# Optimization experiments

Hardware: AMD Instinct MI355X
Metric: run time of the kernel (lower is better)

The kernel has to match this reference:

```python
import jax, jax.numpy as jnp
import numpy as np

INPUT_DIM = 2048
LATENT_DIM = 16384
K = 64
BATCH = 8192


def setup_inputs() -> dict:
    key = jax.random.key(0)
    kx, kw, kbe, kbd = jax.random.split(key, 4)
    x = jax.random.normal(kx, (BATCH, INPUT_DIM), dtype=jnp.float32)
    # torch nn.Linear default init: U(-1/sqrt(fan_in), 1/sqrt(fan_in))
    lim_e = 1.0 / np.sqrt(INPUT_DIM)
    W_enc = jax.random.uniform(kw, (LATENT_DIM, INPUT_DIM), minval=-lim_e, maxval=lim_e, dtype=jnp.float32)
    b_enc = jax.random.uniform(kbe, (LATENT_DIM,), minval=-lim_e, maxval=lim_e, dtype=jnp.float32)
    # decoder weight tied at init to encoder.weight.T -> shape [INPUT_DIM, LATENT_DIM]
    W_dec = W_enc.T
    lim_d = 1.0 / np.sqrt(LATENT_DIM)
    b_dec = jax.random.uniform(kbd, (INPUT_DIM,), minval=-lim_d, maxval=lim_d, dtype=jnp.float32)
    return {"x": x, "W_enc": W_enc, "b_enc": b_enc, "W_dec": W_dec, "b_dec": b_dec}


def reference(x, W_enc, b_enc, W_dec, b_dec):
    # encode: [B, D] @ [D, L] + [L] -> [B, L]
    pre_acts = jax.nn.relu(x @ W_enc.T + b_enc)
    # top-k over latent dim
    topk_vals, topk_idx = jax.lax.top_k(pre_acts, K)          # [B, K]
    # scatter top-k values into a zero latent tensor
    rows = jnp.arange(pre_acts.shape[0])[:, None]             # [B, 1]
    z = jnp.zeros_like(pre_acts).at[rows, topk_idx].set(topk_vals)
    # decode: [B, L] @ [L, D] + [D]
    x_hat = z @ W_dec.T + b_dec
    return (x_hat, z)
```

## Files before the change

kernel.cpp:

```cpp
#include <hip/hip_runtime.h>
#include <cstdint>
#include <cstddef>


#define BATCH  8192
#define IN_DIM 2048
#define LAT    16384
#define TOPK   64

typedef __attribute__((ext_vector_type(8))) _Float16  f16x8;
typedef __attribute__((ext_vector_type(4))) _Float16  f16x4;
typedef __attribute__((ext_vector_type(4))) float     f32x4;
typedef __attribute__((ext_vector_type(8))) unsigned short us8;

#define GLOAD16(gp, lp) __builtin_amdgcn_global_load_lds(                     \
    (const __attribute__((address_space(1))) void*)(gp),                      \
    (__attribute__((address_space(3))) void*)(lp), 16, 0, 0)

__global__ __launch_bounds__(256) void conv_tile(
    const float* __restrict__ X, const float* __restrict__ Wm,
    _Float16* __restrict__ Xt, _Float16* __restrict__ Wt,
    _Float16* __restrict__ Wd)
{
  __shared__ _Float16 l[4096];
  const int t = blockIdx.x;
  const float* src;
  _Float16* dst;
  int grow0 = -1, gcol0 = 0;
  if (t < 4096) {
    src = X + ((size_t)(t >> 6) * 128) * IN_DIM + (t & 63) * 32;
    dst = Xt + (size_t)t * 4096;
  } else {
    const int u = t - 4096;
    src = Wm + ((size_t)(u >> 6) * 128) * IN_DIM + (u & 63) * 32;
    dst = Wt + (size_t)u * 4096;
    grow0 = (u >> 6) * 128;
    gcol0 = (u & 63) * 32;
  }
  const int tid = threadIdx.x;
#pragma unroll
  for (int i = 0; i < 4; ++i) {
    const int q = tid + i * 256;
    const int row = q >> 3, f4 = q & 7;
    const float4 v = *reinterpret_cast<const float4*>(src + (size_t)row * IN_DIM + f4 * 4);
    f16x4 hv;
    hv[0] = (_Float16)v.x; hv[1] = (_Float16)v.y;
    hv[2] = (_Float16)v.z; hv[3] = (_Float16)v.w;
    *reinterpret_cast<f16x4*>(&l[(f4 >> 1) * 1024 + row * 8 + (f4 & 1) * 4]) = hv;
    if (grow0 >= 0)
      *reinterpret_cast<f16x4*>(
          &Wd[(size_t)(grow0 + row) * IN_DIM + gcol0 + f4 * 4]) = hv;
  }
  __syncthreads();
#pragma unroll
  for (int i = 0; i < 2; ++i) {
    const int q = tid + i * 256;
    *reinterpret_cast<us8*>(&dst[(size_t)q * 8]) =
        *reinterpret_cast<const us8*>(&l[q * 8]);
  }
}

#define WAITV(N) asm volatile("s_waitcnt vmcnt(" #N ")" ::: "memory")
#define WAITL do { asm volatile("s_waitcnt lgkmcnt(0)" ::: "memory");         \
                   __builtin_amdgcn_sched_barrier(0); } while (0)
#define BAR __builtin_amdgcn_s_barrier()

#define STAGE_A(par, bufus, t1) do {                                          \
  GLOAD16(At + ((size_t)(bm * 2 + 0) * 64 + 2 * (t1) + (par)) * 4096 + tid8,  \
          &lds[(bufus) + (par) * 8192 + tid8]);                               \
  GLOAD16(At + ((size_t)(bm * 2 + 1) * 64 + 2 * (t1) + (par)) * 4096 + tid8,  \
          &lds[(bufus) + (par) * 8192 + 4096 + tid8]);                        \
} while (0)
#define STAGE_B(par, bufus, t1) do {                                          \
  GLOAD16(Bt + ((size_t)(bn * 2 + 0) * 64 + 2 * (t1) + (par)) * 4096 + tid8,  \
          &lds[(bufus) + 16384 + (par) * 8192 + tid8]);                       \
  GLOAD16(Bt + ((size_t)(bn * 2 + 1) * 64 + 2 * (t1) + (par)) * 4096 + tid8,  \
          &lds[(bufus) + 16384 + (par) * 8192 + 4096 + tid8]);                \
} while (0)

#define LDA4(D, par, bufus, fbase) do {                                       \
  const int _b = (bufus) + (par) * 8192 + wr * 4096 + kg * 1024 + r16 * 8;    \
  _Pragma("unroll") for (int f = 0; f < 4; ++f)                               \
    D[f] = *reinterpret_cast<const f16x8*>(&lds[_b + ((fbase) + f) * 128]);   \
} while (0)
#define LDB4(D, par, bufus) do {                                              \
  const int _b = (bufus) + 16384 + (par) * 8192 + (wc >> 1) * 4096            \
               + kg * 1024 + (wc & 1) * 512 + r16 * 8;                        \
  _Pragma("unroll") for (int g = 0; g < 4; ++g)                               \
    D[g] = *reinterpret_cast<const f16x8*>(&lds[_b + g * 128]);               \
} while (0)

#define MFMA16(fbase, A4, B4) do {                                            \
  __builtin_amdgcn_s_setprio(1);                                              \
  _Pragma("unroll") for (int f = 0; f < 4; ++f)                               \
    _Pragma("unroll") for (int g = 0; g < 4; ++g)                             \
      acc[(fbase) + f][g] = __builtin_amdgcn_mfma_f32_16x16x32_f16(           \
          A4[f], B4[g], acc[(fbase) + f][g], 0, 0, 0);                        \
  __builtin_amdgcn_s_setprio(0); } while (0)

__global__ __launch_bounds__(512, 2) void encode_f16(
    const _Float16* __restrict__ At,
    const _Float16* __restrict__ Bt,
    const float* __restrict__ bias,
    float* __restrict__ C)
{
  __shared__ _Float16 lds[65536];
  const int tid  = threadIdx.x;
  const int lane = tid & 63, wid = tid >> 6;
  const int wr = wid >> 2, wc = wid & 3;
  const int r16 = lane & 15, kg = lane >> 4;
  const int tid8 = tid * 8;

  const int bid = blockIdx.x;
  const int swz = (bid & 7) * 256 + (bid >> 3);
  const int bn = swz & 63, bm = swz >> 6;

  f32x4 acc[8][4];
#pragma unroll
  for (int i = 0; i < 8; ++i)
#pragma unroll
    for (int j = 0; j < 4; ++j) acc[i][j] = (f32x4)0.f;

  f16x8 a0[4], a1[4], bb[4];

  STAGE_A(0, 0, 0);
  STAGE_B(0, 0, 0);
  STAGE_A(1, 0, 0);
  STAGE_B(1, 0, 0);
  WAITV(4);
  BAR;

#pragma unroll 2
  for (int t = 0; t < 31; ++t) {
    const int cur = (t & 1) * 32768, nxt = cur ^ 32768;
    LDA4(a0, 0, cur, 0);
    LDB4(bb, 0, cur);
    STAGE_A(0, nxt, t + 1);
    BAR; WAITL;
    MFMA16(0, a0, bb);
    BAR;
    LDA4(a1, 0, cur, 4);
    STAGE_B(0, nxt, t + 1);
    WAITV(4);
    BAR; WAITL;
    MFMA16(4, a1, bb);
    BAR;
    LDA4(a0, 1, cur, 0);
    LDB4(bb, 1, cur);
    STAGE_A(1, nxt, t + 1);
    STAGE_B(1, nxt, t + 1);
    BAR; WAITL;
    MFMA16(0, a0, bb);
    BAR;
    LDA4(a1, 1, cur, 4);
    WAITV(4);
    BAR; WAITL;
    MFMA16(4, a1, bb);
    BAR;
  }

  {
    const int cur = 32768;
    LDA4(a0, 0, cur, 0);
    LDB4(bb, 0, cur);
    BAR; WAITL;
    MFMA16(0, a0, bb);
    BAR;
    LDA4(a1, 0, cur, 4);
    WAITV(0);
    BAR; WAITL;
    MFMA16(4, a1, bb);
    BAR;
    LDA4(a0, 1, cur, 0);
    LDB4(bb, 1, cur);
    BAR; WAITL;
    MFMA16(0, a0, bb);
    BAR;
    LDA4(a1, 1, cur, 4);
    WAITL;
    MFMA16(4, a1, bb);
  }

  const int row0 = bm * 256 + wr * 128 + (lane >> 4) * 4;
  const int col0 = bn * 256 + wc * 64 + r16;
#pragma unroll
  for (int fj = 0; fj < 4; ++fj) {
    const float bv = bias[col0 + fj * 16];
#pragma unroll
    for (int fi = 0; fi < 8; ++fi) {
#pragma unroll
      for (int q = 0; q < 4; ++q) {
        const float tv = acc[fi][fj][q] + bv;
        C[(size_t)(row0 + fi * 16 + q) * LAT + col0 + fj * 16] = tv > 0.f ? tv : 0.f;
      }
    }
  }
}

#define REFINE_WIN 0.01f
#define MAXMID 96

__global__ __launch_bounds__(256) void topk_decode(
    float* __restrict__ Z,
    const float* __restrict__ X,
    const float* __restrict__ Wm,
    const float* __restrict__ benc,
    const _Float16* __restrict__ Wd,
    const float* __restrict__ b_dec,
    float* __restrict__ Xhat)
{
  const int row = blockIdx.x;
  const int tid = threadIdx.x;
  float* zrow = Z + (size_t)row * LAT;
  const float* xrow = X + (size_t)row * IN_DIM;

  float v[64];
#pragma unroll
  for (int i = 0; i < 16; ++i) {
    const float4 t = *reinterpret_cast<const float4*>(&zrow[(tid << 2) + (i << 10)]);
    v[i * 4 + 0] = t.x; v[i * 4 + 1] = t.y; v[i * 4 + 2] = t.z; v[i * 4 + 3] = t.w;
  }

  __shared__ int hist[256];
  __shared__ int sbuf[256];
  __shared__ int s_bin, s_krnext;
  uint32_t prefix = 0, mask = 0;
  int kr = TOPK;
  for (int p = 3; p >= 2; --p) {
    hist[tid] = 0;
    __syncthreads();
#pragma unroll
    for (int i = 0; i < 64; ++i) {
      const uint32_t u = __float_as_uint(v[i]);
      if ((u & mask) == prefix) atomicAdd(&hist[(u >> (p * 8)) & 255], 1);
    }
    __syncthreads();
    sbuf[tid] = hist[tid];
    for (int s = 1; s < 256; s <<= 1) {
      __syncthreads();
      const int y = (tid + s < 256) ? sbuf[tid + s] : 0;
      __syncthreads();
      sbuf[tid] += y;
    }
    __syncthreads();
    const int suf  = sbuf[tid];
    const int sufn = (tid < 255) ? sbuf[tid + 1] : 0;
    if (suf >= kr && sufn < kr) { s_bin = tid; s_krnext = kr - sufn; }
    __syncthreads();
    prefix |= (uint32_t)s_bin << (p * 8);
    mask   |= 0xFFu << (p * 8);
    kr = s_krnext;
    __syncthreads();
  }

  const float blo = __uint_as_float(prefix);
  const float bhi = __uint_as_float(prefix + 0x10000u);
  const float thi = bhi + REFINE_WIN;
  const float wlo = blo - REFINE_WIN;

  __shared__ int   s_cnt, s_mc;
  __shared__ int   s_mi[MAXMID];
  __shared__ float s_mv[MAXMID];
  __shared__ int   s_oi[TOPK];
  __shared__ float s_ov[TOPK];
  if (tid == 0) { s_cnt = 0; s_mc = 0; }
  __syncthreads();

#pragma unroll
  for (int i = 0; i < 16; ++i) {
    const int ebase = (tid << 2) + (i << 10);
    float4 ov;
    float* op = reinterpret_cast<float*>(&ov);
#pragma unroll
    for (int q = 0; q < 4; ++q) {
      const float val = v[i * 4 + q];
      float o = 0.f;
      if (val > thi) {
        o = val;
        const int pz = atomicAdd(&s_cnt, 1);
        s_oi[pz] = ebase + q;
        s_ov[pz] = val;
      } else if (val >= wlo) {
        const int pe = atomicAdd(&s_mc, 1);
        if (pe < MAXMID) { s_mi[pe] = ebase + q; s_mv[pe] = val; }
      }
      op[q] = o;
    }
    *reinterpret_cast<float4*>(&zrow[ebase]) = ov;
  }
  __syncthreads();

  const int mc = (s_mc < MAXMID) ? s_mc : MAXMID;
  const int m  = TOPK - s_cnt;

  __shared__ double s_ev[MAXMID];
  {
    const int wv = tid >> 6, ln = tid & 63;
    for (int j = wv; j < mc; j += 4) {
      const float* wr = Wm + (size_t)s_mi[j] * IN_DIM;
      const int k0 = ln * 32;
      double p = 0.0;
#pragma unroll
      for (int k = 0; k < 32; ++k)
        p = fma((double)xrow[k0 + k], (double)wr[k0 + k], p);
#pragma unroll
      for (int s = 32; s > 0; s >>= 1) p += __shfl_xor(p, s);
      if (ln == 0) s_ev[j] = p + (double)benc[s_mi[j]];
    }
  }
  __syncthreads();

  if (tid == 0) {
    const int base = s_cnt;
    for (int r = 0; r < m; ++r) {
      int bj = -1;
      for (int j = 0; j < mc; ++j) {
        if (s_ev[j] < -1e290) continue;
        if (bj < 0 || s_ev[j] > s_ev[bj] ||
            (s_ev[j] == s_ev[bj] && s_mi[j] < s_mi[bj])) bj = j;
      }
      if (bj < 0) break;
      zrow[s_mi[bj]] = s_mv[bj];
      s_oi[base + r] = s_mi[bj];
      s_ov[base + r] = s_mv[bj];
      s_ev[bj] = -1e300;
    }
  }
  __syncthreads();

  const int d = tid * 8;
  float4 acc0 = *reinterpret_cast<const float4*>(&b_dec[d]);
  float4 acc1 = *reinterpret_cast<const float4*>(&b_dec[d + 4]);
#pragma unroll 4
  for (int k = 0; k < TOPK; ++k) {
    const float s = s_ov[k];
    const f16x8 wv8 = *reinterpret_cast<const f16x8*>(
        &Wd[(size_t)s_oi[k] * IN_DIM + d]);
    acc0.x = fmaf(s, (float)wv8[0], acc0.x);
    acc0.y = fmaf(s, (float)wv8[1], acc0.y);
    acc0.z = fmaf(s, (float)wv8[2], acc0.z);
    acc0.w = fmaf(s, (float)wv8[3], acc0.w);
    acc1.x = fmaf(s, (float)wv8[4], acc1.x);
    acc1.y = fmaf(s, (float)wv8[5], acc1.y);
    acc1.z = fmaf(s, (float)wv8[6], acc1.z);
    acc1.w = fmaf(s, (float)wv8[7], acc1.w);
  }
  float* xp = &Xhat[(size_t)row * IN_DIM + d];
  *reinterpret_cast<float4*>(xp) = acc0;
  *reinterpret_cast<float4*>(xp + 4) = acc1;
}

constexpr int BMf = 128, BNf = 128, BKf = 16;

__global__ __launch_bounds__(256) void encode_gemm_f64(
    const float* __restrict__ A, const float* __restrict__ B,
    const float* __restrict__ bias, float* __restrict__ C)
{
  __shared__ float As[BKf][BMf + 4];
  __shared__ float Bs[BKf][BNf + 4];
  const int tid = threadIdx.x;
  const int tx = tid & 15, ty = tid >> 4;
  const int block_n = blockIdx.x * BNf, block_m = blockIdx.y * BMf;
  double acc[8][8];
#pragma unroll
  for (int i = 0; i < 8; ++i)
#pragma unroll
    for (int j = 0; j < 8; ++j) acc[i][j] = 0.0;
  const int lr = tid >> 2, lc = tid & 3;
  for (int k0 = 0; k0 < IN_DIM; k0 += BKf) {
    __syncthreads();
#pragma unroll
    for (int it = 0; it < 2; ++it) {
      const int r = lr + it * 64;
      const float4 va = *reinterpret_cast<const float4*>(&A[(size_t)(block_m + r) * IN_DIM + k0 + lc * 4]);
      As[lc * 4 + 0][r] = va.x; As[lc * 4 + 1][r] = va.y;
      As[lc * 4 + 2][r] = va.z; As[lc * 4 + 3][r] = va.w;
      const float4 vb = *reinterpret_cast<const float4*>(&B[(size_t)(block_n + r) * IN_DIM + k0 + lc * 4]);
      Bs[lc * 4 + 0][r] = vb.x; Bs[lc * 4 + 1][r] = vb.y;
      Bs[lc * 4 + 2][r] = vb.z; Bs[lc * 4 + 3][r] = vb.w;
    }
    __syncthreads();
#pragma unroll
    for (int k = 0; k < BKf; ++k) {
      const float4 a0 = *reinterpret_cast<const float4*>(&As[k][ty * 8]);
      const float4 a1 = *reinterpret_cast<const float4*>(&As[k][ty * 8 + 4]);
      const float4 b0 = *reinterpret_cast<const float4*>(&Bs[k][tx * 8]);
      const float4 b1 = *reinterpret_cast<const float4*>(&Bs[k][tx * 8 + 4]);
      const double a[8] = {(double)a0.x, (double)a0.y, (double)a0.z, (double)a0.w,
                           (double)a1.x, (double)a1.y, (double)a1.z, (double)a1.w};
      const double b[8] = {(double)b0.x, (double)b0.y, (double)b0.z, (double)b0.w,
                           (double)b1.x, (double)b1.y, (double)b1.z, (double)b1.w};
#pragma unroll
      for (int i = 0; i < 8; ++i)
#pragma unroll
        for (int j = 0; j < 8; ++j) acc[i][j] = fma(a[i], b[j], acc[i][j]);
    }
  }
  float bv[8];
#pragma unroll
  for (int j = 0; j < 8; ++j) bv[j] = bias[block_n + tx * 8 + j];
#pragma unroll
  for (int i = 0; i < 8; ++i) {
    const int row = block_m + ty * 8 + i;
    float o[8];
#pragma unroll
    for (int j = 0; j < 8; ++j) {
      const double s = acc[i][j] + (double)bv[j];
      o[j] = (float)(s > 0.0 ? s : 0.0);
    }
    float* cp = &C[(size_t)row * LAT + block_n + tx * 8];
    *reinterpret_cast<float4*>(cp)     = make_float4(o[0], o[1], o[2], o[3]);
    *reinterpret_cast<float4*>(cp + 4) = make_float4(o[4], o[5], o[6], o[7]);
  }
}

__global__ __launch_bounds__(256) void topk_fallback(
    float* __restrict__ Z, const float* __restrict__ X,
    const float* __restrict__ Wm, const float* __restrict__ benc,
    int* __restrict__ idx_out, float* __restrict__ val_out)
{
  const int row = blockIdx.x;
  const int tid = threadIdx.x;
  float* zrow = Z + (size_t)row * LAT;
  const float* xrow = X + (size_t)row * IN_DIM;
  float v[64];
#pragma unroll
  for (int i = 0; i < 16; ++i) {
    const float4 t = *reinterpret_cast<const float4*>(&zrow[(tid << 2) + (i << 10)]);
    v[i * 4 + 0] = t.x; v[i * 4 + 1] = t.y; v[i * 4 + 2] = t.z; v[i * 4 + 3] = t.w;
  }
  __shared__ int hist[256];
  __shared__ int sbuf[256];
  __shared__ int s_bin, s_krnext;
  uint32_t prefix = 0, mask = 0;
  int kr = TOPK;
  for (int p = 3; p >= 0; --p) {
    hist[tid] = 0;
    __syncthreads();
#pragma unroll
    for (int i = 0; i < 64; ++i) {
      const uint32_t u = __float_as_uint(v[i]);
      if ((u & mask) == prefix) atomicAdd(&hist[(u >> (p * 8)) & 255], 1);
    }
    __syncthreads();
    sbuf[tid] = hist[tid];
    for (int s = 1; s < 256; s <<= 1) {
      __syncthreads();
      const int y = (tid + s < 256) ? sbuf[tid + s] : 0;
      __syncthreads();
      sbuf[tid] += y;
    }
    __syncthreads();
    const int suf  = sbuf[tid];
    const int sufn = (tid < 255) ? sbuf[tid + 1] : 0;
    if (suf >= kr && sufn < kr) { s_bin = tid; s_krnext = kr - sufn; }
    __syncthreads();
    prefix |= (uint32_t)s_bin << (p * 8);
    mask   |= 0xFFu << (p * 8);
    kr = s_krnext;
    __syncthreads();
  }
  const uint32_t tbits = prefix;
  const int need_eq = kr;
  __shared__ int s_cnt, s_eqcnt;
  __shared__ int s_eqidx[512];
  if (tid == 0) { s_cnt = 0; s_eqcnt = 0; }
  __syncthreads();
#pragma unroll
  for (int i = 0; i < 16; ++i) {
    const int ebase = (tid << 2) + (i << 10);
    float4 ov;
    float* op = reinterpret_cast<float*>(&ov);
#pragma unroll
    for (int q = 0; q < 4; ++q) {
      const float val = v[i * 4 + q];
      const uint32_t u = __float_as_uint(val);
      float o = 0.f;
      if (u > tbits) {
        o = val;
        const int pz = atomicAdd(&s_cnt, 1);
        idx_out[row * TOPK + pz] = ebase + q;
        val_out[row * TOPK + pz] = val;
      } else if (u == tbits) {
        const int pe = atomicAdd(&s_eqcnt, 1);
        if (pe < 512) s_eqidx[pe] = ebase + q;
      }
      op[q] = o;
    }
    *reinterpret_cast<float4*>(&zrow[ebase]) = ov;
  }
  __syncthreads();
  __shared__ double rbuf[256];
  __shared__ double s_ev[8];
  const int ec_all = (s_eqcnt < 512) ? s_eqcnt : 512;
  const bool refine = (ec_all > need_eq) && (ec_all <= 8);
  if (refine) {
    for (int j = 0; j < ec_all; ++j) {
      const float* wr = Wm + (size_t)s_eqidx[j] * IN_DIM;
      double p = 0.0;
      for (int k = tid; k < IN_DIM; k += 256)
        p = fma((double)xrow[k], (double)wr[k], p);
      rbuf[tid] = p;
      __syncthreads();
      for (int s = 128; s > 0; s >>= 1) {
        if (tid < s) rbuf[tid] += rbuf[tid + s];
        __syncthreads();
      }
      if (tid == 0) s_ev[j] = rbuf[0] + (double)benc[s_eqidx[j]];
      __syncthreads();
    }
  }
  if (tid == 0) {
    const int base = s_cnt;
    const float tval = __uint_as_float(tbits);
    if (refine) {
      bool used[8] = {};
      for (int r = 0; r < need_eq; ++r) {
        int bj = -1;
        for (int j = 0; j < ec_all; ++j) {
          if (used[j]) continue;
          if (bj < 0) { bj = j; continue; }
          const bool better = (s_ev[j] > s_ev[bj]) ||
                              (s_ev[j] == s_ev[bj] && s_eqidx[j] < s_eqidx[bj]);
          if (better) bj = j;
        }
        used[bj] = true;
        const int best = s_eqidx[bj];
        zrow[best] = tval;
        idx_out[row * TOPK + base + r] = best;
        val_out[row * TOPK + base + r] = tval;
      }
    } else {
      for (int r = 0; r < need_eq; ++r) {
        int best = 0x7FFFFFFF, bj = -1;
        for (int j = 0; j < ec_all; ++j)
          if (s_eqidx[j] < best) { best = s_eqidx[j]; bj = j; }
        s_eqidx[bj] = 0x7FFFFFFF;
        zrow[best] = tval;
        idx_out[row * TOPK + base + r] = best;
        val_out[row * TOPK + base + r] = tval;
      }
    }
  }
}

__global__ __launch_bounds__(256) void decode_kernel(
    const float* __restrict__ Wrows, const float* __restrict__ b_dec,
    const int* __restrict__ idx_in, const float* __restrict__ val_in,
    float* __restrict__ Xhat)
{
  const int row = blockIdx.x;
  const int tid = threadIdx.x;
  __shared__ int s_idx[TOPK];
  __shared__ float s_val[TOPK];
  if (tid < TOPK) {
    s_idx[tid] = idx_in[row * TOPK + tid];
    s_val[tid] = val_in[row * TOPK + tid];
  }
  __syncthreads();

  const int d = tid * 8;
  float4 acc0 = *reinterpret_cast<const float4*>(&b_dec[d]);
  float4 acc1 = *reinterpret_cast<const float4*>(&b_dec[d + 4]);

  for (int k = 0; k < TOPK; ++k) {
    const float s = s_val[k];
    const float* wr = &Wrows[(size_t)s_idx[k] * IN_DIM + d];
    const float4 w0 = *reinterpret_cast<const float4*>(wr);
    const float4 w1 = *reinterpret_cast<const float4*>(wr + 4);
    acc0.x = fmaf(s, w0.x, acc0.x);
    acc0.y = fmaf(s, w0.y, acc0.y);
    acc0.z = fmaf(s, w0.z, acc0.z);
    acc0.w = fmaf(s, w0.w, acc0.w);
    acc1.x = fmaf(s, w1.x, acc1.x);
    acc1.y = fmaf(s, w1.y, acc1.y);
    acc1.z = fmaf(s, w1.z, acc1.z);
    acc1.w = fmaf(s, w1.w, acc1.w);
  }
  float* xp = &Xhat[(size_t)row * IN_DIM + d];
  *reinterpret_cast<float4*>(xp) = acc0;
  *reinterpret_cast<float4*>(xp + 4) = acc1;
}

extern "C" void kernel_launch(void* const* d_in, const int* in_sizes, int n_in,
                              void* d_out, int out_size, void* d_ws, size_t ws_size,
                              hipStream_t stream) {
  const float* x     = (const float*)d_in[0];
  const float* W_enc = (const float*)d_in[1];
  const float* b_enc = (const float*)d_in[2];
  const float* W_dec = (const float*)d_in[3];
  const float* b_dec = (const float*)d_in[4];
  (void)W_dec; (void)in_sizes; (void)n_in; (void)out_size;

  float* xhat = (float*)d_out;
  float* z    = xhat + (size_t)BATCH * IN_DIM;

  int*   idx_ws = (int*)d_ws;
  float* val_ws = (float*)((char*)d_ws + (size_t)BATCH * TOPK * 4);

  const size_t NEED = 4194304ull + 33554432ull + 67108864ull + 67108864ull;

  if (ws_size >= NEED) {
    _Float16* Xt = (_Float16*)((char*)d_ws + 4194304ull);
    _Float16* Wt = Xt + 16777216ull;
    _Float16* Wd = Wt + 33554432ull;
    conv_tile<<<12288, 256, 0, stream>>>(x, W_enc, Xt, Wt, Wd);
    encode_f16<<<2048, 512, 0, stream>>>(Xt, Wt, b_enc, z);
    topk_decode<<<BATCH, 256, 0, stream>>>(z, x, W_enc, b_enc, Wd, b_dec, xhat);
  } else {
    encode_gemm_f64<<<dim3(LAT / BNf, BATCH / BMf), 256, 0, stream>>>(x, W_enc, b_enc, z);
    topk_fallback<<<BATCH, 256, 0, stream>>>(z, x, W_enc, b_enc, idx_ws, val_ws);
    decode_kernel<<<BATCH, 256, 0, stream>>>(W_enc, b_dec, idx_ws, val_ws, xhat);
  }
}
```

Before: 1.216 ms.

## Compact above-threshold encoder outputs into per-row candidate lists for top-k

The encoder epilogue no longer writes the dense pre-activation matrix. It appends values above a fixed threshold (1.0) to per-row candidate buffers using global atomics. z is zero-filled by a memset, and a new top-k kernel radix-selects from the short candidate list, writes only the 64 winners, and decodes. This removes the full 512MB read-back of z and the dense scan in top-k. In exchange it adds atomic contention in the GEMM epilogue, relies on the threshold suiting the activation distribution, and keeps a slow per-row exact recompute fallback when a row's candidate count is out of range.

```diff
diff --git a/kernel.cpp b/kernel.cpp
--- a/kernel.cpp
+++ b/kernel.cpp
@@ -7,6 +7,8 @@
 #define IN_DIM 2048
 #define LAT    16384
 #define TOPK   64
+#define CAP    1024
+#define T0F    1.0f
 
 typedef __attribute__((ext_vector_type(8))) _Float16  f16x8;
 typedef __attribute__((ext_vector_type(4))) _Float16  f16x4;
@@ -102,7 +104,10 @@
     const _Float16* __restrict__ At,
     const _Float16* __restrict__ Bt,
     const float* __restrict__ bias,
-    float* __restrict__ C)
+    float* __restrict__ Cw,
+    int* __restrict__ ccnt,
+    int* __restrict__ ccidx,
+    float* __restrict__ ccval)
 {
   __shared__ _Float16 lds[65536];
   const int tid  = threadIdx.x;
@@ -190,8 +195,18 @@
     for (int fi = 0; fi < 8; ++fi) {
 #pragma unroll
       for (int q = 0; q < 4; ++q) {
-        const float tv = acc[fi][fj][q] + bv;
-        C[(size_t)(row0 + fi * 16 + q) * LAT + col0 + fj * 16] = tv > 0.f ? tv : 0.f;
+        const float t0 = acc[fi][fj][q] + bv;
+        const float tv = t0 > 0.f ? t0 : 0.f;
+        if (Cw)
+          Cw[(size_t)(row0 + fi * 16 + q) * LAT + col0 + fj * 16] = tv;
+        if (ccnt && tv > T0F) {
+          const int r = row0 + fi * 16 + q;
+          const int pos = atomicAdd(&ccnt[r], 1);
+          if (pos < CAP) {
+            ccidx[(size_t)r * CAP + pos] = col0 + fj * 16;
+            ccval[(size_t)r * CAP + pos] = tv;
+          }
+        }
       }
     }
   }
@@ -200,13 +215,219 @@
 #define REFINE_WIN 0.01f
 #define MAXMID 96
 
-__global__ __launch_bounds__(256) void topk_decode(
+__global__ __launch_bounds__(256) void topk_cand(
+    const int* __restrict__ ccnt, const int* __restrict__ ccidx,
+    const float* __restrict__ ccval,
     float* __restrict__ Z,
     const float* __restrict__ X,
     const float* __restrict__ Wm,
     const float* __restrict__ benc,
     const _Float16* __restrict__ Wd,
     const float* __restrict__ b_dec,
+    float* __restrict__ Xhat)
+{
+  const int row = blockIdx.x;
+  const int tid = threadIdx.x;
+  float* zrow = Z + (size_t)row * LAT;
+  const float* xrow = X + (size_t)row * IN_DIM;
+
+  __shared__ float lv[CAP];
+  __shared__ int   li[CAP];
+  __shared__ int hist[256], sbuf[256];
+  __shared__ int s_bin, s_krnext, s_bad;
+  __shared__ int s_cnt, s_mc;
+  __shared__ int   s_mi[MAXMID];
+  __shared__ float s_mv[MAXMID];
+  __shared__ int   s_oi[TOPK];
+  __shared__ float s_ov[TOPK];
+  __shared__ double s_ev[MAXMID];
+
+  const int n = ccnt[row];
+  bool fast = (n >= TOPK && n <= CAP);
+  float thi = 0.f, wlo = 0.f;
+
+  if (fast) {
+    for (int i = tid; i < n; i += 256) {
+      lv[i] = ccval[(size_t)row * CAP + i];
+      li[i] = ccidx[(size_t)row * CAP + i];
+    }
+    if (tid == 0) s_bad = 0;
+    __syncthreads();
+    uint32_t prefix = 0, mask = 0;
+    int kr = TOPK;
+    for (int p = 3; p >= 2; --p) {
+      hist[tid] = 0;
+      __syncthreads();
+      for (int i = tid; i < n; i += 256) {
+        const uint32_t u = __float_as_uint(lv[i]);
+        if ((u & mask) == prefix) atomicAdd(&hist[(u >> (p * 8)) & 255], 1);
+      }
+      __syncthreads();
+      sbuf[tid] = hist[tid];
+      for (int s = 1; s < 256; s <<= 1) {
+        __syncthreads();
+        const int y = (tid + s < 256) ? sbuf[tid + s] : 0;
+        __syncthreads();
+        sbuf[tid] += y;
+      }
+      __syncthreads();
+      const int suf  = sbuf[tid];
+      const int sufn = (tid < 255) ? sbuf[tid + 1] : 0;
+      if (suf >= kr && sufn < kr) { s_bin = tid; s_krnext = kr - sufn; }
+      __syncthreads();
+      prefix |= (uint32_t)s_bin << (p * 8);
+      mask   |= 0xFFu << (p * 8);
+      kr = s_krnext;
+      __syncthreads();
+    }
+    const float blo = __uint_as_float(prefix);
+    const float bhi = __uint_as_float(prefix + 0x10000u);
+    thi = bhi + REFINE_WIN;
+    wlo = blo - REFINE_WIN;
+    if (wlo <= T0F + 0.001f) fast = false;
+  }
+
+  if (fast) {
+    if (tid == 0) { s_cnt = 0; s_mc = 0; }
+    __syncthreads();
+    for (int i = tid; i < n; i += 256) {
+      const float val = lv[i];
+      if (val > thi) {
+        const int p = atomicAdd(&s_cnt, 1);
+        if (p < TOPK) { s_oi[p] = li[i]; s_ov[p] = val; } else s_bad = 1;
+      } else if (val >= wlo) {
+        const int p = atomicAdd(&s_mc, 1);
+        if (p < MAXMID) { s_mi[p] = li[i]; s_mv[p] = val; } else s_bad = 1;
+      }
+    }
+    __syncthreads();
+    if (s_bad) fast = false;
+  }
+
+  if (!fast) {
+    for (int j = tid; j < LAT; j += 256) {
+      const float* wr2 = Wm + (size_t)j * IN_DIM;
+      float a0 = 0.f, a1 = 0.f, a2 = 0.f, a3 = 0.f;
+      for (int k = 0; k < IN_DIM; k += 4) {
+        const float4 xv = *reinterpret_cast<const float4*>(&xrow[k]);
+        const float4 wv = *reinterpret_cast<const float4*>(&wr2[k]);
+        a0 = fmaf(xv.x, wv.x, a0); a1 = fmaf(xv.y, wv.y, a1);
+        a2 = fmaf(xv.z, wv.z, a2); a3 = fmaf(xv.w, wv.w, a3);
+      }
+      const float dot = ((a0 + a1) + (a2 + a3)) + benc[j];
+      zrow[j] = dot > 0.f ? dot : 0.f;
+    }
+    __syncthreads();
+    uint32_t prefix = 0, mask = 0;
+    int kr = TOPK;
+    for (int p = 3; p >= 0; --p) {
+      hist[tid] = 0;
+      __syncthreads();
+      for (int i = tid; i < LAT; i += 256) {
+        const uint32_t u = __float_as_uint(zrow[i]);
+        if ((u & mask) == prefix) atomicAdd(&hist[(u >> (p * 8)) & 255], 1);
+      }
+      __syncthreads();
+      sbuf[tid] = hist[tid];
+      for (int s = 1; s < 256; s <<= 1) {
+        __syncthreads();
+        const int y = (tid + s < 256) ? sbuf[tid + s] : 0;
+        __syncthreads();
+        sbuf[tid] += y;
+      }
+      __syncthreads();
+      const int suf  = sbuf[tid];
+      const int sufn = (tid < 255) ? sbuf[tid + 1] : 0;
+      if (suf >= kr && sufn < kr) { s_bin = tid; s_krnext = kr - sufn; }
+      __syncthreads();
+      prefix |= (uint32_t)s_bin << (p * 8);
+      mask   |= 0xFFu << (p * 8);
+      kr = s_krnext;
+      __syncthreads();
+    }
+    const uint32_t tbits = prefix;
+    if (tid == 0) { s_cnt = 0; s_mc = 0; }
+    __syncthreads();
+    for (int i = tid; i < LAT; i += 256) {
+      const float val = zrow[i];
+      const uint32_t u = __float_as_uint(val);
+      float o = 0.f;
+      if (u > tbits) {
+        o = val;
+        const int p = atomicAdd(&s_cnt, 1);
+        s_oi[p] = i; s_ov[p] = val;
+      } else if (u == tbits) {
+        const int p = atomicAdd(&s_mc, 1);
+        if (p < MAXMID) { s_mi[p] = i; s_mv[p] = val; }
+      }
+      zrow[i] = o;
+    }
+    __syncthreads();
+  }
+
+  const int mc = (s_mc < MAXMID) ? s_mc : MAXMID;
+  const int m  = TOPK - s_cnt;
+  {
+    const int wv = tid >> 6, ln = tid & 63;
+    for (int j = wv; j < mc; j += 4) {
+      const float* wr2 = Wm + (size_t)s_mi[j] * IN_DIM;
+      const int k0 = ln * 32;
+      double p = 0.0;
+#pragma unroll
+      for (int k = 0; k < 32; ++k)
+        p = fma((double)xrow[k0 + k], (double)wr2[k0 + k], p);
+#pragma unroll
+      for (int s = 32; s > 0; s >>= 1) p += __shfl_xor(p, s);
+      if (ln == 0) s_ev[j] = p + (double)benc[s_mi[j]];
+    }
+  }
+  __syncthreads();
+
+  if (tid == 0) {
+    const int base = s_cnt;
+    for (int r = 0; r < m; ++r) {
+      int bj = -1;
+      for (int j = 0; j < mc; ++j) {
+        if (s_ev[j] < -1e290) continue;
+        if (bj < 0 || s_ev[j] > s_ev[bj] ||
+            (s_ev[j] == s_ev[bj] && s_mi[j] < s_mi[bj])) bj = j;
+      }
+      if (bj < 0) break;
+      s_oi[base + r] = s_mi[bj];
+      s_ov[base + r] = s_mv[bj];
+      s_ev[bj] = -1e300;
+    }
+  }
+  __syncthreads();
+
+  if (tid < TOPK) zrow[s_oi[tid]] = s_ov[tid];
+
+  const int d = tid * 8;
+  float4 acc0 = *reinterpret_cast<const float4*>(&b_dec[d]);
+  float4 acc1 = *reinterpret_cast<const float4*>(&b_dec[d + 4]);
+#pragma unroll 4
+  for (int k = 0; k < TOPK; ++k) {
+    const float s = s_ov[k];
+    const f16x8 wv8 = *reinterpret_cast<const f16x8*>(
+        &Wd[(size_t)s_oi[k] * IN_DIM + d]);
+    acc0.x = fmaf(s, (float)wv8[0], acc0.x);
+    acc0.y = fmaf(s, (float)wv8[1], acc0.y);
+    acc0.z = fmaf(s, (float)wv8[2], acc0.z);
+    acc0.w = fmaf(s, (float)wv8[3], acc0.w);
+    acc1.x = fmaf(s, (float)wv8[4], acc1.x);
+    acc1.y = fmaf(s, (float)wv8[5], acc1.y);
+    acc1.z = fmaf(s, (float)wv8[6], acc1.z);
+    acc1.w = fmaf(s, (float)wv8[7], acc1.w);
+  }
+  float* xp = &Xhat[(size_t)row * IN_DIM + d];
+  *reinterpret_cast<float4*>(xp) = acc0;
+  *reinterpret_cast<float4*>(xp + 4) = acc1;
+}
+
+__global__ __launch_bounds__(256) void topk_decode(
+    float* __restrict__ Z, const float* __restrict__ X,
+    const float* __restrict__ Wm, const float* __restrict__ benc,
+    const _Float16* __restrict__ Wd, const float* __restrict__ b_dec,
     float* __restrict__ Xhat)
 {
   const int row = blockIdx.x;
@@ -598,15 +819,36 @@
   int*   idx_ws = (int*)d_ws;
   float* val_ws = (float*)((char*)d_ws + (size_t)BATCH * TOPK * 4);
 
-  const size_t NEED = 4194304ull + 33554432ull + 67108864ull + 67108864ull;
-
-  if (ws_size >= NEED) {
-    _Float16* Xt = (_Float16*)((char*)d_ws + 4194304ull);
-    _Float16* Wt = Xt + 16777216ull;
-    _Float16* Wd = Wt + 33554432ull;
-    conv_tile<<<12288, 256, 0, stream>>>(x, W_enc, Xt, Wt, Wd);
-    encode_f16<<<2048, 512, 0, stream>>>(Xt, Wt, b_enc, z);
-    topk_decode<<<BATCH, 256, 0, stream>>>(z, x, W_enc, b_enc, Wd, b_dec, xhat);
+  const size_t OFF_XT = 4ull * 1024 * 1024;
+  const size_t OFF_WT = OFF_XT + 32ull * 1024 * 1024;
+  const size_t OFF_WD = OFF_WT + 64ull * 1024 * 1024;
+  const size_t OFF_CV = OFF_WD + 64ull * 1024 * 1024;
+  const size_t OFF_CI = OFF_CV + 32ull * 1024 * 1024;
+  const size_t OFF_CN = OFF_CI + 32ull * 1024 * 1024;
+  const size_t NEED_FAST = OFF_CN + (size_t)BATCH * 4;
+  const size_t NEED_MID  = OFF_CV;
+
+  if (ws_size >= NEED_MID) {
+    _Float16* Xt = (_Float16*)((char*)d_ws + OFF_XT);
+    _Float16* Wt = (_Float16*)((char*)d_ws + OFF_WT);
+    _Float16* Wd = (_Float16*)((char*)d_ws + OFF_WD);
+    if (ws_size >= NEED_FAST) {
+      float* ccval = (float*)((char*)d_ws + OFF_CV);
+      int*   ccidx = (int*)((char*)d_ws + OFF_CI);
+      int*   ccnt  = (int*)((char*)d_ws + OFF_CN);
+      hipMemsetAsync(z, 0, (size_t)BATCH * LAT * 4, stream);
+      hipMemsetAsync(ccnt, 0, (size_t)BATCH * 4, stream);
+      conv_tile<<<12288, 256, 0, stream>>>(x, W_enc, Xt, Wt, Wd);
+      encode_f16<<<2048, 512, 0, stream>>>(Xt, Wt, b_enc,
+                                           nullptr, ccnt, ccidx, ccval);
+      topk_cand<<<BATCH, 256, 0, stream>>>(ccnt, ccidx, ccval, z, x, W_enc,
+                                           b_enc, Wd, b_dec, xhat);
+    } else {
+      conv_tile<<<12288, 256, 0, stream>>>(x, W_enc, Xt, Wt, Wd);
+      encode_f16<<<2048, 512, 0, stream>>>(Xt, Wt, b_enc,
+                                           z, nullptr, nullptr, nullptr);
+      topk_decode<<<BATCH, 256, 0, stream>>>(z, x, W_enc, b_enc, Wd, b_dec, xhat);
+    }
   } else {
     encode_gemm_f64<<<dim3(LAT / BNf, BATCH / BMf), 256, 0, stream>>>(x, W_enc, b_enc, z);
     topk_fallback<<<BATCH, 256, 0, stream>>>(z, x, W_enc, b_enc, idx_ws, val_ws);
```

After: 2.196 ms. 1.81x slower.
